# Kernel tuning notes

Measured on AMD Instinct MI355X. Metric: run time of the kernel, lower is better.

## Reference

```python
import jax, jax.numpy as jnp
import numpy as np

N_NODES = 100000
N_EDGES = 1600000
D_IN = 64
D_H = 64
N_CLS = 2


def setup_inputs() -> dict:
    key = jax.random.key(0)
    ks = jax.random.split(key, 12)
    s = 0.05
    return {
        "features": jax.random.normal(ks[0], (N_NODES, D_IN), dtype=jnp.float32),
        "edge_index": jax.random.randint(ks[1], (2, N_EDGES), 0, N_NODES, dtype=jnp.int64),
        # SAGE layer 1: Linear(2*D_IN, D_H)
        "W1": jax.random.normal(ks[2], (D_H, 2 * D_IN), dtype=jnp.float32) * s,
        "b1": jnp.zeros((D_H,), dtype=jnp.float32),
        # SAGE layer 2: Linear(2*D_H, D_H)
        "W2": jax.random.normal(ks[3], (D_H, 2 * D_H), dtype=jnp.float32) * s,
        "b2": jnp.zeros((D_H,), dtype=jnp.float32),
        # classifier: Linear(D_H, D_H//2) -> ReLU -> Linear(D_H//2, N_CLS)
        "Wc1": jax.random.normal(ks[4], (D_H // 2, D_H), dtype=jnp.float32) * s,
        "bc1": jnp.zeros((D_H // 2,), dtype=jnp.float32),
        "Wc2": jax.random.normal(ks[5], (N_CLS, D_H // 2), dtype=jnp.float32) * s,
        "bc2": jnp.zeros((N_CLS,), dtype=jnp.float32),
    }


def _sage_layer(x, edge_index, W, b):
    # gather src features, scatter-mean into dst, concat with self, linear
    src, dst = edge_index[0], edge_index[1]
    n = x.shape[0]
    ones = jnp.ones(src.shape[0], dtype=x.dtype)
    deg = jax.ops.segment_sum(ones, dst, num_segments=n)
    deg = jnp.maximum(deg, 1.0)  # clamp(min=1)
    neigh = jax.ops.segment_sum(x[src], dst, num_segments=n) / deg[:, None]
    combined = jnp.concatenate([x, neigh], axis=-1)  # [n, 2*d]
    return combined @ W.T + b


def reference(features, edge_index, W1, b1, W2, b2, Wc1, bc1, Wc2, bc2):
    # two SAGE layers with ReLU (dropout = identity at eval)
    x = jax.nn.relu(_sage_layer(features, edge_index, W1, b1))
    x = jax.nn.relu(_sage_layer(x, edge_index, W2, b2))
    # classifier head (embedding_projection unused when return_embeddings=False)
    h = jax.nn.relu(x @ Wc1.T + bc1)
    logits = h @ Wc2.T + bc2
    return logits
```

## Files before the change

### kernel.cpp

```cpp
#include <hip/hip_runtime.h>

#define D 64
#define TSCAN 1024

__device__ __forceinline__ float bcast(float v, int l) {
    return __uint_as_float(__builtin_amdgcn_readlane(__float_as_uint(v), l));
}

__global__ void __launch_bounds__(256) hist_kernel(
    const int* __restrict__ dst, int* __restrict__ cnt, int E)
{
    int t = blockIdx.x * blockDim.x + threadIdx.x;
    int st = gridDim.x * blockDim.x;
    for (int e = t; e < E; e += st) atomicAdd(&cnt[dst[e]], 1);
}

__global__ void __launch_bounds__(TSCAN) partial_kernel(
    const int* __restrict__ cnt, int* __restrict__ partials, int n)
{
    __shared__ int red[TSCAN];
    int i = blockIdx.x * TSCAN + threadIdx.x;
    red[threadIdx.x] = (i < n) ? cnt[i] : 0;
    __syncthreads();
    for (int off = TSCAN / 2; off > 0; off >>= 1) {
        if (threadIdx.x < off) red[threadIdx.x] += red[threadIdx.x + off];
        __syncthreads();
    }
    if (threadIdx.x == 0) partials[blockIdx.x] = red[0];
}

__global__ void __launch_bounds__(128) scanp_kernel(
    const int* __restrict__ partials, int* __restrict__ blockoff, int nb)
{
    __shared__ int s[128];
    int t = threadIdx.x;
    int orig = (t < nb) ? partials[t] : 0;
    s[t] = orig;
    __syncthreads();
    for (int off = 1; off < 128; off <<= 1) {
        int v = (t >= off) ? s[t - off] : 0;
        __syncthreads();
        s[t] += v;
        __syncthreads();
    }
    if (t < nb) blockoff[t] = s[t] - orig;
}

__global__ void __launch_bounds__(TSCAN) rowptr_kernel(
    const int* __restrict__ cnt, const int* __restrict__ blockoff,
    int* __restrict__ rowptr, int* __restrict__ cursor, int n)
{
    __shared__ int s[TSCAN];
    int b = blockIdx.x;
    int i = b * TSCAN + threadIdx.x;
    int v = (i < n) ? cnt[i] : 0;
    s[threadIdx.x] = v;
    __syncthreads();
    for (int off = 1; off < TSCAN; off <<= 1) {
        int x = (threadIdx.x >= off) ? s[threadIdx.x - off] : 0;
        __syncthreads();
        s[threadIdx.x] += x;
        __syncthreads();
    }
    if (i < n) {
        int excl = blockoff[b] + s[threadIdx.x] - v;
        rowptr[i] = excl;
        cursor[i] = excl;
        if (i == n - 1) rowptr[n] = excl + v;
    }
}

__global__ void __launch_bounds__(256) fill_kernel(
    const int* __restrict__ src, const int* __restrict__ dst,
    int* __restrict__ cursor, int* __restrict__ adj, int E)
{
    int t = blockIdx.x * blockDim.x + threadIdx.x;
    int st = gridDim.x * blockDim.x;
    for (int e = t; e < E; e += st) {
        int p = atomicAdd(&cursor[dst[e]], 1);
        adj[p] = src[e];
    }
}

template <bool HEAD>
__global__ void __launch_bounds__(512, 4) sage_kernel(
    const float* __restrict__ x,
    const int*   __restrict__ rowptr,
    const int*   __restrict__ adj,
    const float* __restrict__ W,
    const float* __restrict__ b,
    const float* __restrict__ Wc1,
    const float* __restrict__ bc1,
    const float* __restrict__ Wc2,
    const float* __restrict__ bc2,
    float*       __restrict__ out,
    int n)
{
    extern __shared__ float smem[];
    float4* Wt4 = (float4*)smem;
    float*  Wt  = smem;
    float*  bs  = smem + 8192;
    float*  wc1t = bs + 64;
    float*  w2s  = wc1t + 2048;
    float*  bc1s = w2s + 64;
    float*  bc2s = bc1s + 32;

    for (int d = threadIdx.x; d < 64 * 128; d += blockDim.x) {
        int k4 = d >> 8;
        int j  = (d >> 2) & 63;
        int kk = d & 3;
        Wt[d] = W[j * 128 + k4 * 4 + kk];
    }
    if (threadIdx.x < 64) bs[threadIdx.x] = b[threadIdx.x];
    if (HEAD) {
        for (int d = threadIdx.x; d < 32 * 64; d += blockDim.x) {
            int k = d >> 5, l = d & 31;
            wc1t[d] = Wc1[l * 64 + k];
        }
        if (threadIdx.x < 64) w2s[threadIdx.x] = Wc2[threadIdx.x];
        if (threadIdx.x < 32) bc1s[threadIdx.x] = bc1[threadIdx.x];
        if (threadIdx.x < 2)  bc2s[threadIdx.x] = bc2[threadIdx.x];
    }
    __syncthreads();

    int lane = threadIdx.x & 63;
    int wid  = (blockIdx.x * blockDim.x + threadIdx.x) >> 6;
    int nw   = (gridDim.x * blockDim.x) >> 6;
    for (int node = wid; node < n; node += nw) {
        int ro = rowptr[node], re = rowptr[node + 1];
        float acc0 = 0.f, acc1 = 0.f;
        int i = ro;
        for (; i + 8 <= re; i += 8) {
            int s0 = adj[i+0], s1 = adj[i+1], s2 = adj[i+2], s3 = adj[i+3];
            int s4 = adj[i+4], s5 = adj[i+5], s6 = adj[i+6], s7 = adj[i+7];
            float v0 = x[(size_t)s0 * D + lane];
            float v1 = x[(size_t)s1 * D + lane];
            float v2 = x[(size_t)s2 * D + lane];
            float v3 = x[(size_t)s3 * D + lane];
            float v4 = x[(size_t)s4 * D + lane];
            float v5 = x[(size_t)s5 * D + lane];
            float v6 = x[(size_t)s6 * D + lane];
            float v7 = x[(size_t)s7 * D + lane];
            acc0 += (v0 + v1) + (v2 + v3);
            acc1 += (v4 + v5) + (v6 + v7);
        }
        for (; i < re; ++i) acc0 += x[(size_t)adj[i] * D + lane];
        float acc = acc0 + acc1;
        float av = acc / fmaxf((float)(re - ro), 1.0f);
        float xv = x[(size_t)node * D + lane];

        float sum = bs[lane];
        #pragma unroll
        for (int k4 = 0; k4 < 16; ++k4) {
            float4 w = Wt4[k4 * 64 + lane];
            sum = fmaf(bcast(xv, 4 * k4 + 0), w.x, sum);
            sum = fmaf(bcast(xv, 4 * k4 + 1), w.y, sum);
            sum = fmaf(bcast(xv, 4 * k4 + 2), w.z, sum);
            sum = fmaf(bcast(xv, 4 * k4 + 3), w.w, sum);
        }
        #pragma unroll
        for (int k4 = 16; k4 < 32; ++k4) {
            float4 w = Wt4[k4 * 64 + lane];
            int kk = 4 * (k4 - 16);
            sum = fmaf(bcast(av, kk + 0), w.x, sum);
            sum = fmaf(bcast(av, kk + 1), w.y, sum);
            sum = fmaf(bcast(av, kk + 2), w.z, sum);
            sum = fmaf(bcast(av, kk + 3), w.w, sum);
        }
        float x2 = fmaxf(sum, 0.0f);

        if (!HEAD) {
            out[(size_t)node * D + lane] = x2;
        } else {
            int l = lane & 31;
            float h = bc1s[l];
            #pragma unroll
            for (int k = 0; k < 64; ++k)
                h = fmaf(bcast(x2, k), wc1t[k * 32 + l], h);
            h = fmaxf(h, 0.0f);
            float p0 = (lane < 32) ? h * w2s[l]      : 0.0f;
            float p1 = (lane < 32) ? h * w2s[32 + l] : 0.0f;
            #pragma unroll
            for (int off = 1; off < 64; off <<= 1) {
                p0 += __shfl_xor(p0, off, 64);
                p1 += __shfl_xor(p1, off, 64);
            }
            if (lane == 0) {
                out[(size_t)node * 2 + 0] = p0 + bc2s[0];
                out[(size_t)node * 2 + 1] = p1 + bc2s[1];
            }
        }
    }
}

extern "C" void kernel_launch(void* const* d_in, const int* in_sizes, int n_in,
                              void* d_out, int out_size, void* d_ws, size_t ws_size,
                              hipStream_t stream)
{
    const float* feat = (const float*)d_in[0];
    const int*   eidx = (const int*)d_in[1];
    const float* W1   = (const float*)d_in[2];
    const float* b1   = (const float*)d_in[3];
    const float* W2   = (const float*)d_in[4];
    const float* b2   = (const float*)d_in[5];
    const float* Wc1  = (const float*)d_in[6];
    const float* bc1  = (const float*)d_in[7];
    const float* Wc2  = (const float*)d_in[8];
    const float* bc2  = (const float*)d_in[9];

    int n = in_sizes[0] / D;
    int E = in_sizes[1] / 2;
    const int* src = eidx;
    const int* dst = eidx + E;

    int*   cnt      = (int*)d_ws;
    int*   partials = cnt + n;
    int*   blockoff = partials + 128;
    int*   rowptr   = blockoff + 128;
    int*   cursor   = rowptr + n + 1;
    int*   adj      = cursor + n;
    float* x1       = (float*)(adj + E);

    int nb = (n + TSCAN - 1) / TSCAN;

    hipMemsetAsync(cnt, 0, (size_t)n * sizeof(int), stream);
    hist_kernel<<<6250, 256, 0, stream>>>(dst, cnt, E);
    partial_kernel<<<nb, TSCAN, 0, stream>>>(cnt, partials, n);
    scanp_kernel<<<1, 128, 0, stream>>>(partials, blockoff, nb);
    rowptr_kernel<<<nb, TSCAN, 0, stream>>>(cnt, blockoff, rowptr, cursor, n);
    fill_kernel<<<6250, 256, 0, stream>>>(src, dst, cursor, adj, E);

    size_t lds1 = (8192 + 64) * sizeof(float);
    sage_kernel<false><<<512, 512, lds1, stream>>>(
        feat, rowptr, adj, W1, b1, nullptr, nullptr, nullptr, nullptr, x1, n);

    size_t lds2 = (8192 + 64 + 2048 + 64 + 32 + 2) * sizeof(float);
    sage_kernel<true><<<512, 512, lds2, stream>>>(
        x1, rowptr, adj, W2, b2, Wc1, bc1, Wc2, bc2, (float*)d_out, n);
}
```

Before: 917.7 us.

## Store node features in bf16 and gather half-rows per lane group

Converts input features and the intermediate layer output to packed bf16, so the neighbor gather reads half as many bytes per row. Each wave now gathers two neighbors at once, with each half-wave loading a 32-bit pair of bf16 values, and neighbor indices are preloaded into lanes and broadcast with shuffles. Launch bounds and grid size are doubled for occupancy. This adds a conversion kernel and loses precision in the features and hidden activations.

```diff
diff --git a/kernel.cpp b/kernel.cpp
--- a/kernel.cpp
+++ b/kernel.cpp
@@ -3,8 +3,28 @@
 #define D 64
 #define TSCAN 1024
 
-__device__ __forceinline__ float bcast(float v, int l) {
+typedef unsigned int  u32;
+typedef unsigned short u16;
+
+__device__ __forceinline__ float bcastf(float v, int l) {
     return __uint_as_float(__builtin_amdgcn_readlane(__float_as_uint(v), l));
+}
+__device__ __forceinline__ u32 f2bf(float f) {
+    u32 u = __float_as_uint(f);
+    return (u + 0x7fffu + ((u >> 16) & 1u)) >> 16;
+}
+__device__ __forceinline__ float bflo(u32 v) { return __uint_as_float(v << 16); }
+__device__ __forceinline__ float bfhi(u32 v) { return __uint_as_float(v & 0xffff0000u); }
+
+__global__ void __launch_bounds__(256) tobf16_kernel(
+    const float* __restrict__ x, u32* __restrict__ xh, int npairs)
+{
+    int t = blockIdx.x * blockDim.x + threadIdx.x;
+    int st = gridDim.x * blockDim.x;
+    for (int i = t; i < npairs; i += st) {
+        float2 v = ((const float2*)x)[i];
+        xh[i] = f2bf(v.x) | (f2bf(v.y) << 16);
+    }
 }
 
 __global__ void __launch_bounds__(256) hist_kernel(
@@ -83,8 +103,8 @@
 }
 
 template <bool HEAD>
-__global__ void __launch_bounds__(512, 4) sage_kernel(
-    const float* __restrict__ x,
+__global__ void __launch_bounds__(512, 8) sage_kernel(
+    const u16*   __restrict__ xh,
     const int*   __restrict__ rowptr,
     const int*   __restrict__ adj,
     const float* __restrict__ W,
@@ -93,7 +113,7 @@
     const float* __restrict__ bc1,
     const float* __restrict__ Wc2,
     const float* __restrict__ bc2,
-    float*       __restrict__ out,
+    void*        __restrict__ out_,
     int n)
 {
     extern __shared__ float smem[];
@@ -123,60 +143,92 @@
     }
     __syncthreads();
 
+    const u32* xh32 = (const u32*)xh;
     int lane = threadIdx.x & 63;
+    int g    = lane >> 5;
+    int m    = lane & 31;
     int wid  = (blockIdx.x * blockDim.x + threadIdx.x) >> 6;
     int nw   = (gridDim.x * blockDim.x) >> 6;
+
     for (int node = wid; node < n; node += nw) {
         int ro = rowptr[node], re = rowptr[node + 1];
-        float acc0 = 0.f, acc1 = 0.f;
+        int deg = re - ro;
+        int av_idx = (ro + lane < re) ? adj[ro + lane] : 0;
+        float xv = __uint_as_float(((u32)xh[(size_t)node * 64 + lane]) << 16);
+
+        float accx = 0.f, accy = 0.f;
+        int ilim = min(re, ro + 64);
         int i = ro;
-        for (; i + 8 <= re; i += 8) {
-            int s0 = adj[i+0], s1 = adj[i+1], s2 = adj[i+2], s3 = adj[i+3];
-            int s4 = adj[i+4], s5 = adj[i+5], s6 = adj[i+6], s7 = adj[i+7];
-            float v0 = x[(size_t)s0 * D + lane];
-            float v1 = x[(size_t)s1 * D + lane];
-            float v2 = x[(size_t)s2 * D + lane];
-            float v3 = x[(size_t)s3 * D + lane];
-            float v4 = x[(size_t)s4 * D + lane];
-            float v5 = x[(size_t)s5 * D + lane];
-            float v6 = x[(size_t)s6 * D + lane];
-            float v7 = x[(size_t)s7 * D + lane];
-            acc0 += (v0 + v1) + (v2 + v3);
-            acc1 += (v4 + v5) + (v6 + v7);
-        }
-        for (; i < re; ++i) acc0 += x[(size_t)adj[i] * D + lane];
-        float acc = acc0 + acc1;
-        float av = acc / fmaxf((float)(re - ro), 1.0f);
-        float xv = x[(size_t)node * D + lane];
+        #pragma unroll 2
+        for (; i + 8 <= ilim; i += 8) {
+            int c = i - ro;
+            int e0 = __shfl(av_idx, c + 0 + g, 64);
+            int e1 = __shfl(av_idx, c + 2 + g, 64);
+            int e2 = __shfl(av_idx, c + 4 + g, 64);
+            int e3 = __shfl(av_idx, c + 6 + g, 64);
+            u32 v0 = xh32[(size_t)e0 * 32 + m];
+            u32 v1 = xh32[(size_t)e1 * 32 + m];
+            u32 v2 = xh32[(size_t)e2 * 32 + m];
+            u32 v3 = xh32[(size_t)e3 * 32 + m];
+            accx += (bflo(v0) + bflo(v1)) + (bflo(v2) + bflo(v3));
+            accy += (bfhi(v0) + bfhi(v1)) + (bfhi(v2) + bfhi(v3));
+        }
+        int t = ilim - i;
+        if (t) {
+            int c = i - ro, w = ilim - ro - 1;
+            int c0 = min(c + 0 + g, w), c1 = min(c + 2 + g, w);
+            int c2 = min(c + 4 + g, w), c3 = min(c + 6 + g, w);
+            int e0 = __shfl(av_idx, c0, 64);
+            int e1 = __shfl(av_idx, c1, 64);
+            int e2 = __shfl(av_idx, c2, 64);
+            int e3 = __shfl(av_idx, c3, 64);
+            u32 v0 = xh32[(size_t)e0 * 32 + m];
+            u32 v1 = xh32[(size_t)e1 * 32 + m];
+            u32 v2 = xh32[(size_t)e2 * 32 + m];
+            u32 v3 = xh32[(size_t)e3 * 32 + m];
+            float m0 = (0 + g < t) ? 1.f : 0.f;
+            float m1 = (2 + g < t) ? 1.f : 0.f;
+            float m2 = (4 + g < t) ? 1.f : 0.f;
+            float m3 = (6 + g < t) ? 1.f : 0.f;
+            accx += bflo(v0) * m0 + bflo(v1) * m1 + bflo(v2) * m2 + bflo(v3) * m3;
+            accy += bfhi(v0) * m0 + bfhi(v1) * m1 + bfhi(v2) * m2 + bfhi(v3) * m3;
+        }
+        for (int ii = ro + 64; ii < re; ++ii) {
+            u32 v = xh32[(size_t)adj[ii] * 32 + m];
+            if (g == 0) { accx += bflo(v); accy += bfhi(v); }
+        }
+        accx += __shfl_xor(accx, 32, 64);
+        accy += __shfl_xor(accy, 32, 64);
+        float inv = 1.0f / fmaxf((float)deg, 1.0f);
+        accx *= inv; accy *= inv;
 
         float sum = bs[lane];
         #pragma unroll
         for (int k4 = 0; k4 < 16; ++k4) {
             float4 w = Wt4[k4 * 64 + lane];
-            sum = fmaf(bcast(xv, 4 * k4 + 0), w.x, sum);
-            sum = fmaf(bcast(xv, 4 * k4 + 1), w.y, sum);
-            sum = fmaf(bcast(xv, 4 * k4 + 2), w.z, sum);
-            sum = fmaf(bcast(xv, 4 * k4 + 3), w.w, sum);
+            sum = fmaf(bcastf(xv, 4 * k4 + 0), w.x, sum);
+            sum = fmaf(bcastf(xv, 4 * k4 + 1), w.y, sum);
+            sum = fmaf(bcastf(xv, 4 * k4 + 2), w.z, sum);
+            sum = fmaf(bcastf(xv, 4 * k4 + 3), w.w, sum);
         }
         #pragma unroll
-        for (int k4 = 16; k4 < 32; ++k4) {
-            float4 w = Wt4[k4 * 64 + lane];
-            int kk = 4 * (k4 - 16);
-            sum = fmaf(bcast(av, kk + 0), w.x, sum);
-            sum = fmaf(bcast(av, kk + 1), w.y, sum);
-            sum = fmaf(bcast(av, kk + 2), w.z, sum);
-            sum = fmaf(bcast(av, kk + 3), w.w, sum);
+        for (int k4 = 0; k4 < 16; ++k4) {
+            float4 w = Wt4[(16 + k4) * 64 + lane];
+            sum = fmaf(bcastf(accx, 2 * k4 + 0), w.x, sum);
+            sum = fmaf(bcastf(accy, 2 * k4 + 0), w.y, sum);
+            sum = fmaf(bcastf(accx, 2 * k4 + 1), w.z, sum);
+            sum = fmaf(bcastf(accy, 2 * k4 + 1), w.w, sum);
         }
         float x2 = fmaxf(sum, 0.0f);
 
         if (!HEAD) {
-            out[(size_t)node * D + lane] = x2;
+            ((u16*)out_)[(size_t)node * 64 + lane] = (u16)f2bf(x2);
         } else {
             int l = lane & 31;
             float h = bc1s[l];
             #pragma unroll
             for (int k = 0; k < 64; ++k)
-                h = fmaf(bcast(x2, k), wc1t[k * 32 + l], h);
+                h = fmaf(bcastf(x2, k), wc1t[k * 32 + l], h);
             h = fmaxf(h, 0.0f);
             float p0 = (lane < 32) ? h * w2s[l]      : 0.0f;
             float p1 = (lane < 32) ? h * w2s[32 + l] : 0.0f;
@@ -186,8 +238,9 @@
                 p1 += __shfl_xor(p1, off, 64);
             }
             if (lane == 0) {
-                out[(size_t)node * 2 + 0] = p0 + bc2s[0];
-                out[(size_t)node * 2 + 1] = p1 + bc2s[1];
+                float* outf = (float*)out_;
+                outf[(size_t)node * 2 + 0] = p0 + bc2s[0];
+                outf[(size_t)node * 2 + 1] = p1 + bc2s[1];
             }
         }
     }
@@ -213,16 +266,18 @@
     const int* src = eidx;
     const int* dst = eidx + E;
 
-    int*   cnt      = (int*)d_ws;
-    int*   partials = cnt + n;
-    int*   blockoff = partials + 128;
-    int*   rowptr   = blockoff + 128;
-    int*   cursor   = rowptr + n + 1;
-    int*   adj      = cursor + n;
-    float* x1       = (float*)(adj + E);
+    int* cnt      = (int*)d_ws;
+    int* partials = cnt + n;
+    int* blockoff = partials + 128;
+    int* rowptr   = blockoff + 128;
+    int* cursor   = rowptr + n + 1;
+    int* adj      = cursor + n;
+    u32* featH    = (u32*)(adj + E);
+    u32* x1H      = featH + (size_t)n * 32;
 
     int nb = (n + TSCAN - 1) / TSCAN;
 
+    tobf16_kernel<<<2048, 256, 0, stream>>>(feat, featH, n * 32);
     hipMemsetAsync(cnt, 0, (size_t)n * sizeof(int), stream);
     hist_kernel<<<6250, 256, 0, stream>>>(dst, cnt, E);
     partial_kernel<<<nb, TSCAN, 0, stream>>>(cnt, partials, n);
@@ -231,10 +286,12 @@
     fill_kernel<<<6250, 256, 0, stream>>>(src, dst, cursor, adj, E);
 
     size_t lds1 = (8192 + 64) * sizeof(float);
-    sage_kernel<false><<<512, 512, lds1, stream>>>(
-        feat, rowptr, adj, W1, b1, nullptr, nullptr, nullptr, nullptr, x1, n);
+    sage_kernel<false><<<1024, 512, lds1, stream>>>(
+        (const u16*)featH, rowptr, adj, W1, b1,
+        nullptr, nullptr, nullptr, nullptr, (void*)x1H, n);
 
     size_t lds2 = (8192 + 64 + 2048 + 64 + 32 + 2) * sizeof(float);
-    sage_kernel<true><<<512, 512, lds2, stream>>>(
-        x1, rowptr, adj, W2, b2, Wc1, bc1, Wc2, bc2, (float*)d_out, n);
-}
+    sage_kernel<true><<<1024, 512, lds2, stream>>>(
+        (const u16*)x1H, rowptr, adj, W2, b2,
+        Wc1, bc1, Wc2, bc2, d_out, n);
+}
```

Result: slower. 1.739 ms (+89.5%).
